# Kernel tuning notes

Measured on AMD Instinct MI355X. Metric: run time of the kernel, lower is better.

## Reference

```python
import jax, jax.numpy as jnp
import numpy as np

B, C, H, W = 16, 128, 128, 128
NUM_HEADS, HEAD_DIM = 4, 32
HIDDEN = NUM_HEADS * HEAD_DIM  # 128
GROUPS = 32
EPS = 1e-5


def setup_inputs() -> dict:
    key = jax.random.key(0)
    ks = jax.random.split(key, 6)
    # conv1x1 weights: torch Conv2d weight (out, in, 1, 1) -> stored as (out, in)
    fan_qkv = C
    fan_proj = HIDDEN
    return {
        "x": jax.random.normal(ks[0], (B, C, H, W), dtype=jnp.float32),
        "gn_w": jnp.ones((C,), dtype=jnp.float32),
        "gn_b": jnp.zeros((C,), dtype=jnp.float32),
        "qkv_w": jax.random.normal(ks[1], (3 * HIDDEN, C), dtype=jnp.float32) / np.sqrt(fan_qkv),
        "proj_w": jax.random.normal(ks[2], (C, HIDDEN), dtype=jnp.float32) / np.sqrt(fan_proj),
        "proj_b": jax.random.normal(ks[3], (C,), dtype=jnp.float32) * 0.01,
    }


def reference(x, gn_w, gn_b, qkv_w, proj_w, proj_b):
    b, c, h, w = x.shape
    n = h * w
    residual = x
    # GroupNorm(32 groups), biased variance, affine
    xg = x.reshape(b, GROUPS, c // GROUPS, h, w)
    mu = xg.mean(axis=(2, 3, 4), keepdims=True)
    var = xg.var(axis=(2, 3, 4), keepdims=True)
    xn = ((xg - mu) * jax.lax.rsqrt(var + EPS)).reshape(b, c, h, w)
    xn = xn * gn_w[None, :, None, None] + gn_b[None, :, None, None]
    # 1x1 conv QKV (no bias); channel layout -> (b, 3, heads, head_dim, n)
    qkv = jnp.einsum('oc,bchw->bohw', qkv_w, xn)
    qkv = qkv.reshape(b, 3, NUM_HEADS, HEAD_DIM, n)
    q, k, v = qkv[:, 0], qkv[:, 1], qkv[:, 2]
    q = jax.nn.softmax(q, axis=-1)   # over spatial positions
    k = jax.nn.softmax(k, axis=-2)   # over head_dim
    # context = k @ v^T : (b,h,D,D)
    ctx = jnp.einsum('bhdn,bhen->bhde', k, v)
    # out = context^T @ q : (b,h,D,n)
    out = jnp.einsum('bhde,bhdn->bhen', ctx, q)
    out = out.reshape(b, HIDDEN, h, w)
    # 1x1 conv projection (with bias)
    out = jnp.einsum('co,bohw->bchw', proj_w, out) + proj_b[None, :, None, None]
    return out + residual
```

## Files before the change

### kernel.cpp

```cpp
#include <hip/hip_runtime.h>


#define B_ 16
#define C_ 128
#define N_ 16384

typedef short bf16x8 __attribute__((ext_vector_type(8)));
typedef float f32x4 __attribute__((ext_vector_type(4)));
typedef unsigned u32x2 __attribute__((ext_vector_type(2)));

__device__ __forceinline__ ushort f2bf(float f) {
    union { float f; unsigned u; } v; v.f = f;
    unsigned r = (v.u + 0x7FFFu + ((v.u >> 16) & 1u)) >> 16;
    return (ushort)r;
}
__device__ __forceinline__ float bf2f(unsigned h) {
    union { unsigned u; float f; } v; v.u = h << 16;
    return v.f;
}

__global__ void k_stats(const float* __restrict__ x, const float* __restrict__ gnw,
                        const float* __restrict__ gnb, float* __restrict__ sc,
                        float* __restrict__ bi,
                        const float* __restrict__ qkvw, ushort* __restrict__ wbf) {
    int bg = blockIdx.x;
    if (bg >= 512) {
        int i = (bg - 512) * 1024 + threadIdx.x;
        if (i < 384 * 128) wbf[i] = f2bf(qkvw[i]);
        return;
    }
    const float4* p = (const float4*)(x + (size_t)bg * (4 * N_));
    float s = 0.f, s2 = 0.f;
    for (int i = threadIdx.x; i < N_; i += 1024) {
        float4 v = p[i];
        s  += v.x + v.y + v.z + v.w;
        s2 += v.x * v.x + v.y * v.y + v.z * v.z + v.w * v.w;
    }
    #pragma unroll
    for (int d = 32; d > 0; d >>= 1) { s += __shfl_xor(s, d); s2 += __shfl_xor(s2, d); }
    __shared__ float ls[16], ls2[16];
    int wid = threadIdx.x >> 6, lane = threadIdx.x & 63;
    if (lane == 0) { ls[wid] = s; ls2[wid] = s2; }
    __syncthreads();
    if (threadIdx.x == 0) {
        float S = 0.f, S2 = 0.f;
        #pragma unroll
        for (int i = 0; i < 16; ++i) { S += ls[i]; S2 += ls2[i]; }
        float m = S / 65536.f;
        float var = S2 / 65536.f - m * m;
        float rs = rsqrtf(var + 1e-5f);
        int b = bg >> 5, g = bg & 31;
        #pragma unroll
        for (int i = 0; i < 4; ++i) {
            int c = g * 4 + i;
            float scv = rs * gnw[c];
            sc[b * 128 + c] = scv;
            bi[b * 128 + c] = gnb[c] - m * scv;
        }
    }
}


#define MFMA16(A, Bv, Cc) __builtin_amdgcn_mfma_f32_16x16x32_bf16(A, Bv, Cc, 0, 0, 0)

#define DO_Q(J) do { \
    f32x4 acc = {0.f, 0.f, 0.f, 0.f}; \
    acc = MFMA16(wf[J][0], xb[0], acc); acc = MFMA16(wf[J][1], xb[1], acc); \
    acc = MFMA16(wf[J][2], xb[2], acc); acc = MFMA16(wf[J][3], xb[3], acc); \
    qacc[J][0] += __expf(acc[0]); qacc[J][1] += __expf(acc[1]); \
    qacc[J][2] += __expf(acc[2]); qacc[J][3] += __expf(acc[3]); \
} while (0)

#define DO_K(JLO, H) do { \
    f32x4 aL = {0.f, 0.f, 0.f, 0.f}, aH = {0.f, 0.f, 0.f, 0.f}; \
    aL = MFMA16(wf[JLO][0], xb[0], aL);     aH = MFMA16(wf[(JLO)+1][0], xb[0], aH); \
    aL = MFMA16(wf[JLO][1], xb[1], aL);     aH = MFMA16(wf[(JLO)+1][1], xb[1], aH); \
    aL = MFMA16(wf[JLO][2], xb[2], aL);     aH = MFMA16(wf[(JLO)+1][2], xb[2], aH); \
    aL = MFMA16(wf[JLO][3], xb[3], aL);     aH = MFMA16(wf[(JLO)+1][3], xb[3], aH); \
    float eL0 = __expf(aL[0]), eL1 = __expf(aL[1]), eL2 = __expf(aL[2]), eL3 = __expf(aL[3]); \
    float eH0 = __expf(aH[0]), eH1 = __expf(aH[1]), eH2 = __expf(aH[2]), eH3 = __expf(aH[3]); \
    float s = eL0 + eL1 + eL2 + eL3 + eH0 + eH1 + eH2 + eH3; \
    s += __shfl_xor(s, 16); s += __shfl_xor(s, 32); \
    float rinv = 1.f / s; \
    ksm[H][lg * 4 + 0][nloc] = f2bf(eL0 * rinv); \
    ksm[H][lg * 4 + 1][nloc] = f2bf(eL1 * rinv); \
    ksm[H][lg * 4 + 2][nloc] = f2bf(eL2 * rinv); \
    ksm[H][lg * 4 + 3][nloc] = f2bf(eL3 * rinv); \
    ksm[H][16 + lg * 4 + 0][nloc] = f2bf(eH0 * rinv); \
    ksm[H][16 + lg * 4 + 1][nloc] = f2bf(eH1 * rinv); \
    ksm[H][16 + lg * 4 + 2][nloc] = f2bf(eH2 * rinv); \
    ksm[H][16 + lg * 4 + 3][nloc] = f2bf(eH3 * rinv); \
} while (0)

#define DO_V(J, HV, EB) do { \
    f32x4 acc = {0.f, 0.f, 0.f, 0.f}; \
    acc = MFMA16(wf[J][0], xb[0], acc); acc = MFMA16(wf[J][1], xb[1], acc); \
    acc = MFMA16(wf[J][2], xb[2], acc); acc = MFMA16(wf[J][3], xb[3], acc); \
    vls[HV][(EB) + lg * 4 + 0][nloc] = f2bf(acc[0]); \
    vls[HV][(EB) + lg * 4 + 1][nloc] = f2bf(acc[1]); \
    vls[HV][(EB) + lg * 4 + 2][nloc] = f2bf(acc[2]); \
    vls[HV][(EB) + lg * 4 + 3][nloc] = f2bf(acc[3]); \
} while (0)

__global__ __launch_bounds__(256, 2) void k_main(
    const float* __restrict__ x, const ushort* __restrict__ wbf,
    const float* __restrict__ scA, const float* __restrict__ biA,
    float* __restrict__ qsumP, float* __restrict__ ctxP) {
    int blk = blockIdx.x;
    int b = blk >> 6, nb = blk & 63;
    int tid = threadIdx.x, wid = tid >> 6, lane = tid & 63;
    int l15 = lane & 15, lg = lane >> 4;

    __shared__ __align__(16) ushort xs[4096];
    __shared__ __align__(16) ushort ksm[4][32][40];
    __shared__ __align__(16) ushort vls[4][32][40];

    bf16x8 wf[6][4];
    {
        const ushort* wr = wbf + (size_t)(wid * 96 + l15) * 128 + lg * 8;
        #pragma unroll
        for (int j = 0; j < 6; ++j)
            #pragma unroll
            for (int kc = 0; kc < 4; ++kc)
                wf[j][kc] = *(const bf16x8*)(wr + j * 2048 + kc * 32);
    }

    float qacc[6][4];
    #pragma unroll
    for (int j = 0; j < 6; ++j)
        #pragma unroll
        for (int r = 0; r < 4; ++r) qacc[j][r] = 0.f;
    f32x4 cacc[2][2];
    #pragma unroll
    for (int di = 0; di < 2; ++di)
        #pragma unroll
        for (int ei = 0; ei < 2; ++ei) cacc[di][ei] = (f32x4){0.f, 0.f, 0.f, 0.f};

    const int pk_ = tid & 7, pcb = tid >> 3;
    const float* xrow = x + (size_t)b * (C_ * N_) + nb * 256 + pk_ * 4;
    float scv[4], biv[4];
    #pragma unroll
    for (int i = 0; i < 4; ++i) {
        scv[i] = scA[b * 128 + pcb * 4 + i];
        biv[i] = biA[b * 128 + pcb * 4 + i];
    }
    unsigned boffj[4];
    #pragma unroll
    for (int j = 0; j < 4; ++j) {
        int n = pk_ * 4 + j;
        boffj[j] = (unsigned)(n * 256 + (((pcb >> 1) * 16) ^ ((n & 7) << 4)) + (pcb & 1) * 8);
    }

    float4 vbuf[4];
    #pragma unroll
    for (int i = 0; i < 4; ++i)
        vbuf[i] = *(const float4*)(xrow + (size_t)(pcb * 4 + i) * N_);

    for (int ch = 0; ch < 8; ++ch) {
        __syncthreads();
        unsigned e[4][4];
        #pragma unroll
        for (int i = 0; i < 4; ++i) {
            float s = scv[i], t = biv[i];
            e[i][0] = f2bf(vbuf[i].x * s + t);
            e[i][1] = f2bf(vbuf[i].y * s + t);
            e[i][2] = f2bf(vbuf[i].z * s + t);
            e[i][3] = f2bf(vbuf[i].w * s + t);
        }
        if (ch < 7) {
            #pragma unroll
            for (int i = 0; i < 4; ++i)
                vbuf[i] = *(const float4*)(xrow + (size_t)(pcb * 4 + i) * N_ + (ch + 1) * 32);
        }
        #pragma unroll
        for (int j = 0; j < 4; ++j) {
            u32x2 wj;
            wj.x = e[0][j] | (e[1][j] << 16);
            wj.y = e[2][j] | (e[3][j] << 16);
            *(u32x2*)((char*)xs + boffj[j]) = wj;
        }
        __syncthreads();

        #pragma unroll
        for (int nt = 0; nt < 2; ++nt) {
            int row = nt * 16 + l15;
            bf16x8 xb[4];
            #pragma unroll
            for (int kc = 0; kc < 4; ++kc) {
                unsigned off = (unsigned)(row * 256 +
                    (((kc * 4 + lg) * 16) ^ ((row & 7) << 4)));
                xb[kc] = *(const bf16x8*)((const char*)xs + off);
            }
            int nloc = nt * 16 + l15;

            if (wid == 0) {
                DO_Q(0); DO_Q(1); DO_Q(2); DO_Q(3); DO_Q(4); DO_Q(5);
            } else if (wid == 1) {
                DO_Q(0); DO_Q(1); DO_K(2, 0); DO_K(4, 1);
            } else if (wid == 2) {
                DO_K(0, 2); DO_K(2, 3); DO_V(4, 0, 0); DO_V(5, 0, 16);
            } else {
                DO_V(0, 1, 0); DO_V(1, 1, 16); DO_V(2, 2, 0);
                DO_V(3, 2, 16); DO_V(4, 3, 0); DO_V(5, 3, 16);
            }
        }
        __syncthreads();

        {
            bf16x8 A0 = *(const bf16x8*)&ksm[wid][l15][lg * 8];
            bf16x8 A1 = *(const bf16x8*)&ksm[wid][16 + l15][lg * 8];
            bf16x8 B0 = *(const bf16x8*)&vls[wid][l15][lg * 8];
            bf16x8 B1 = *(const bf16x8*)&vls[wid][16 + l15][lg * 8];
            cacc[0][0] = MFMA16(A0, B0, cacc[0][0]);
            cacc[0][1] = MFMA16(A0, B1, cacc[0][1]);
            cacc[1][0] = MFMA16(A1, B0, cacc[1][0]);
            cacc[1][1] = MFMA16(A1, B1, cacc[1][1]);
        }
    }

    int nq = (wid == 0) ? 6 : (wid == 1 ? 2 : 0);
    #pragma unroll
    for (int j = 0; j < 6; ++j) {
        if (j < nq) {
            #pragma unroll
            for (int r = 0; r < 4; ++r) {
                float s = qacc[j][r];
                s += __shfl_xor(s, 1); s += __shfl_xor(s, 2);
                s += __shfl_xor(s, 4); s += __shfl_xor(s, 8);
                if (l15 == 0)
                    qsumP[(size_t)blk * 128 + (wid * 6 + j) * 16 + lg * 4 + r] = s;
            }
        }
    }
    float* cp = ctxP + (size_t)blk * 4096 + wid * 1024;
    #pragma unroll
    for (int di = 0; di < 2; ++di)
        #pragma unroll
        for (int ei = 0; ei < 2; ++ei)
            #pragma unroll
            for (int r = 0; r < 4; ++r)
                cp[(di * 16 + lg * 4 + r) * 32 + ei * 16 + l15] = cacc[di][ei][r];
}

__global__ void k_red(float* __restrict__ ctxP) {
    int blk = blockIdx.x;
    int b = blk >> 3, sl = blk & 7;
    float* base = ctxP + (size_t)b * 64 * 4096;
    #pragma unroll
    for (int r = 0; r < 2; ++r) {
        int i = sl * 512 + r * 256 + threadIdx.x;
        float s = 0.f;
        for (int q = 0; q < 64; ++q) s += base[(size_t)q * 4096 + i];
        base[i] = s;
    }
}

__global__ void k_comb(const float* __restrict__ ctxP, const float* __restrict__ qsumP,
                       const float* __restrict__ projw, ushort* __restrict__ mpp) {
    int b = blockIdx.x, tid = threadIdx.x;
    __shared__ float ctx[4096];
    __shared__ float qinv[128];
    for (int i = tid; i < 4096; i += 256)
        ctx[i] = ctxP[(size_t)b * 64 * 4096 + i];
    if (tid < 128) {
        float s = 0.f;
        const float* p = qsumP + (size_t)b * 64 * 128 + tid;
        for (int q = 0; q < 64; ++q) s += p[q * 128];
        qinv[tid] = 1.f / s;
    }
    __syncthreads();
    int c = tid >> 1, hd0 = (tid & 1) * 64;
    unsigned ow[32];
    for (int k = 0; k < 64; ++k) {
        int hd = hd0 + k, h = hd >> 5, d = hd & 31;
        const float* pw = projw + c * 128 + h * 32;
        const float* cx = ctx + h * 1024 + d * 32;
        float s = 0.f;
        #pragma unroll 8
        for (int e = 0; e < 32; ++e) s += pw[e] * cx[e];
        s *= qinv[hd];
        ushort bv = f2bf(s);
        if (k & 1) ow[k >> 1] |= ((unsigned)bv) << 16; else ow[k >> 1] = bv;
    }
    ushort* dst = mpp + ((size_t)(b * 128 + c)) * 128 + hd0;
    #pragma unroll
    for (int q = 0; q < 8; ++q) {
        uint4 t; t.x = ow[q * 4]; t.y = ow[q * 4 + 1]; t.z = ow[q * 4 + 2]; t.w = ow[q * 4 + 3];
        ((uint4*)dst)[q] = t;
    }
}

__global__ __launch_bounds__(256) void k_final(
    const ushort* __restrict__ wbf, const ushort* __restrict__ mpp,
    const float* __restrict__ scA, const float* __restrict__ biA,
    const float* __restrict__ projb, const float* __restrict__ x,
    float* __restrict__ out) {
    int blk = blockIdx.x;
    int b = blk >> 8, nb = blk & 255;
    int tid = threadIdx.x, wid = tid >> 6, lane = tid & 63;
    int l15 = lane & 15, lg = lane >> 4;
    int n0 = nb * 64;

    __shared__ __align__(16) char lds[32768];
    ushort* xs   = (ushort*)lds;
    ushort* att  = (ushort*)lds;
    ushort* eqls = (ushort*)(lds + 16384);

    bf16x8 wq[2][4];
    #pragma unroll
    for (int j = 0; j < 2; ++j) {
        const ushort* wr = wbf + (size_t)((wid * 2 + j) * 16 + l15) * 128 + lg * 8;
        #pragma unroll
        for (int kc = 0; kc < 4; ++kc) wq[j][kc] = *(const bf16x8*)(wr + kc * 32);
    }
    bf16x8 bm[2][4];
    #pragma unroll
    for (int ctk = 0; ctk < 2; ++ctk) {
        const ushort* br = mpp + ((size_t)(b * 128 + (wid * 2 + ctk) * 16 + l15)) * 128 + lg * 8;
        #pragma unroll
        for (int kc = 0; kc < 4; ++kc) bm[ctk][kc] = *(const bf16x8*)(br + kc * 32);
    }

    const int pk_ = tid & 15, pcb = tid >> 4;
    float4 xv[8];
    {
        const float* xrow = x + (size_t)b * (C_ * N_) + n0 + pk_ * 4;
        unsigned e[8][4];
        #pragma unroll
        for (int i = 0; i < 8; ++i) {
            int c = pcb * 8 + i;
            float s = scA[b * 128 + c], t = biA[b * 128 + c];
            xv[i] = *(const float4*)(xrow + (size_t)c * N_);
            e[i][0] = f2bf(xv[i].x * s + t);
            e[i][1] = f2bf(xv[i].y * s + t);
            e[i][2] = f2bf(xv[i].z * s + t);
            e[i][3] = f2bf(xv[i].w * s + t);
        }
        #pragma unroll
        for (int j = 0; j < 4; ++j) {
            int n = pk_ * 4 + j;
            uint4 wj;
            wj.x = e[0][j] | (e[1][j] << 16);
            wj.y = e[2][j] | (e[3][j] << 16);
            wj.z = e[4][j] | (e[5][j] << 16);
            wj.w = e[6][j] | (e[7][j] << 16);
            unsigned byte = (unsigned)(n * 256 + ((pcb * 16) ^ ((n & 7) << 4)));
            *(uint4*)((char*)xs + byte) = wj;
        }
    }
    __syncthreads();

    #pragma unroll
    for (int nt = 0; nt < 4; ++nt) {
        int row = nt * 16 + l15;
        bf16x8 xb[4];
        #pragma unroll
        for (int kc = 0; kc < 4; ++kc) {
            unsigned off = (unsigned)(row * 256 + (((kc * 4 + lg) * 16) ^ ((row & 7) << 4)));
            xb[kc] = *(const bf16x8*)((const char*)xs + off);
        }
        #pragma unroll
        for (int j = 0; j < 2; ++j) {
            f32x4 a = {0.f, 0.f, 0.f, 0.f};
            #pragma unroll
            for (int kc = 0; kc < 4; ++kc) a = MFMA16(wq[j][kc], xb[kc], a);
            u32x2 pk;
            pk.x = (unsigned)f2bf(__expf(a[0])) | ((unsigned)f2bf(__expf(a[1])) << 16);
            pk.y = (unsigned)f2bf(__expf(a[2])) | ((unsigned)f2bf(__expf(a[3])) << 16);
            int ot = wid * 2 + j;
            unsigned byte = (unsigned)(row * 256 +
                (((ot * 2 + (lg >> 1)) * 16) ^ ((row & 7) << 4)) + (lg & 1) * 8);
            *(u32x2*)((char*)eqls + byte) = pk;
        }
    }
    __syncthreads();

    #pragma unroll
    for (int nt = 0; nt < 4; ++nt) {
        int row = nt * 16 + l15;
        bf16x8 af[4];
        #pragma unroll
        for (int kc = 0; kc < 4; ++kc) {
            unsigned off = (unsigned)(row * 256 + (((kc * 4 + lg) * 16) ^ ((row & 7) << 4)));
            af[kc] = *(const bf16x8*)((const char*)eqls + off);
        }
        #pragma unroll
        for (int ctk = 0; ctk < 2; ++ctk) {
            f32x4 a = {0.f, 0.f, 0.f, 0.f};
            #pragma unroll
            for (int kc = 0; kc < 4; ++kc) a = MFMA16(af[kc], bm[ctk][kc], a);
            int c = (wid * 2 + ctk) * 16 + l15;
            u32x2 pk;
            pk.x = (unsigned)f2bf(a[0]) | ((unsigned)f2bf(a[1]) << 16);
            pk.y = (unsigned)f2bf(a[2]) | ((unsigned)f2bf(a[3]) << 16);
            unsigned byte = (unsigned)(c * 128 +
                (((nt * 2 + (lg >> 1)) * 16) ^ ((c & 7) << 4)) + (lg & 1) * 8);
            *(u32x2*)((char*)att + byte) = pk;
        }
    }
    __syncthreads();

    {
        size_t obase = (size_t)b * (C_ * N_) + n0 + pk_ * 4;
        #pragma unroll
        for (int i = 0; i < 8; ++i) {
            int c = pcb * 8 + i;
            unsigned byte = (unsigned)(c * 128 +
                (((pk_ >> 1) * 16) ^ ((c & 7) << 4)) + (pk_ & 1) * 8);
            u32x2 pk = *(const u32x2*)((const char*)att + byte);
            float pbv = projb[c];
            f32x4 o4;
            o4[0] = bf2f(pk.x & 0xffffu) + pbv + xv[i].x;
            o4[1] = bf2f(pk.x >> 16)     + pbv + xv[i].y;
            o4[2] = bf2f(pk.y & 0xffffu) + pbv + xv[i].z;
            o4[3] = bf2f(pk.y >> 16)     + pbv + xv[i].w;
            *(f32x4*)(out + obase + (size_t)c * N_) = o4;
        }
    }
}

extern "C" void kernel_launch(void* const* d_in, const int* in_sizes, int n_in,
                              void* d_out, int out_size, void* d_ws, size_t ws_size,
                              hipStream_t stream) {
    const float* x     = (const float*)d_in[0];
    const float* gnw   = (const float*)d_in[1];
    const float* gnb   = (const float*)d_in[2];
    const float* qkvw  = (const float*)d_in[3];
    const float* projw = (const float*)d_in[4];
    const float* projb = (const float*)d_in[5];
    float* out = (float*)d_out;

    char* ws = (char*)d_ws;
    ushort* wbf   = (ushort*)(ws);
    float*  qsumP = (float*)(ws + 102400);
    ushort* mpp   = (ushort*)(ws + 626688);
    float*  sc    = (float*)(ws + 1150976);
    float*  bi    = (float*)(ws + 1159168);
    float*  ctxP  = (float*)(ws + 1167360);

    k_stats<<<560,  1024, 0, stream>>>(x, gnw, gnb, sc, bi, qkvw, wbf);
    k_main <<<1024, 256,  0, stream>>>(x, wbf, sc, bi, qsumP, ctxP);
    k_red  <<<128,  256,  0, stream>>>(ctxP);
    k_comb <<<16,   256,  0, stream>>>(ctxP, qsumP, projw, mpp);
    k_final<<<4096, 256,  0, stream>>>(wbf, mpp, sc, bi, projb, x, out);
}
```

Before: 211.5 us.

## Defer context MFMA past barrier and fold partial reduction into combine kernel

Moves the per-chunk K·V^T context MFMA to the start of the next chunk iteration, removing one block barrier per chunk in the main kernel. Merges the separate partial-context reduction kernel into the combine kernel, which now uses 1024 threads per batch to sum the 64 partials directly into shared memory. This saves a launch and a global round trip, but the reduction now runs on only 16 blocks, and removing the barrier risks a race on the shared staging buffer if it is not double-buffered.

```diff
diff --git a/kernel.cpp b/kernel.cpp
--- a/kernel.cpp
+++ b/kernel.cpp
@@ -102,6 +102,17 @@
     vls[HV][(EB) + lg * 4 + 3][nloc] = f2bf(acc[3]); \
 } while (0)
 
+#define DO_CTX() do { \
+    bf16x8 A0 = *(const bf16x8*)&ksm[wid][l15][lg * 8]; \
+    bf16x8 A1 = *(const bf16x8*)&ksm[wid][16 + l15][lg * 8]; \
+    bf16x8 B0 = *(const bf16x8*)&vls[wid][l15][lg * 8]; \
+    bf16x8 B1 = *(const bf16x8*)&vls[wid][16 + l15][lg * 8]; \
+    cacc[0][0] = MFMA16(A0, B0, cacc[0][0]); \
+    cacc[0][1] = MFMA16(A0, B1, cacc[0][1]); \
+    cacc[1][0] = MFMA16(A1, B0, cacc[1][0]); \
+    cacc[1][1] = MFMA16(A1, B1, cacc[1][1]); \
+} while (0)
+
 __global__ __launch_bounds__(256, 2) void k_main(
     const float* __restrict__ x, const ushort* __restrict__ wbf,
     const float* __restrict__ scA, const float* __restrict__ biA,
@@ -179,6 +190,7 @@
             wj.y = e[2][j] | (e[3][j] << 16);
             *(u32x2*)((char*)xs + boffj[j]) = wj;
         }
+        if (ch > 0) DO_CTX();
         __syncthreads();
 
         #pragma unroll
@@ -204,19 +216,9 @@
                 DO_V(3, 2, 16); DO_V(4, 3, 0); DO_V(5, 3, 16);
             }
         }
-        __syncthreads();
-
-        {
-            bf16x8 A0 = *(const bf16x8*)&ksm[wid][l15][lg * 8];
-            bf16x8 A1 = *(const bf16x8*)&ksm[wid][16 + l15][lg * 8];
-            bf16x8 B0 = *(const bf16x8*)&vls[wid][l15][lg * 8];
-            bf16x8 B1 = *(const bf16x8*)&vls[wid][16 + l15][lg * 8];
-            cacc[0][0] = MFMA16(A0, B0, cacc[0][0]);
-            cacc[0][1] = MFMA16(A0, B1, cacc[0][1]);
-            cacc[1][0] = MFMA16(A1, B0, cacc[1][0]);
-            cacc[1][1] = MFMA16(A1, B1, cacc[1][1]);
-        }
-    }
+    }
+    __syncthreads();
+    DO_CTX();
 
     int nq = (wid == 0) ? 6 : (wid == 1 ? 2 : 0);
     #pragma unroll
@@ -242,26 +244,20 @@
                 cp[(di * 16 + lg * 4 + r) * 32 + ei * 16 + l15] = cacc[di][ei][r];
 }
 
-__global__ void k_red(float* __restrict__ ctxP) {
-    int blk = blockIdx.x;
-    int b = blk >> 3, sl = blk & 7;
-    float* base = ctxP + (size_t)b * 64 * 4096;
-    #pragma unroll
-    for (int r = 0; r < 2; ++r) {
-        int i = sl * 512 + r * 256 + threadIdx.x;
-        float s = 0.f;
-        for (int q = 0; q < 64; ++q) s += base[(size_t)q * 4096 + i];
-        base[i] = s;
-    }
-}
-
-__global__ void k_comb(const float* __restrict__ ctxP, const float* __restrict__ qsumP,
-                       const float* __restrict__ projw, ushort* __restrict__ mpp) {
+__global__ __launch_bounds__(1024) void k_comb(
+    const float* __restrict__ ctxP, const float* __restrict__ qsumP,
+    const float* __restrict__ projw, ushort* __restrict__ mpp) {
     int b = blockIdx.x, tid = threadIdx.x;
     __shared__ float ctx[4096];
     __shared__ float qinv[128];
-    for (int i = tid; i < 4096; i += 256)
-        ctx[i] = ctxP[(size_t)b * 64 * 4096 + i];
+    const float* base = ctxP + (size_t)b * 64 * 4096;
+    #pragma unroll
+    for (int r = 0; r < 4; ++r) {
+        int i = r * 1024 + tid;
+        float s = 0.f;
+        for (int q = 0; q < 64; ++q) s += base[(size_t)q * 4096 + i];
+        ctx[i] = s;
+    }
     if (tid < 128) {
         float s = 0.f;
         const float* p = qsumP + (size_t)b * 64 * 128 + tid;
@@ -269,24 +265,27 @@
         qinv[tid] = 1.f / s;
     }
     __syncthreads();
-    int c = tid >> 1, hd0 = (tid & 1) * 64;
-    unsigned ow[32];
-    for (int k = 0; k < 64; ++k) {
-        int hd = hd0 + k, h = hd >> 5, d = hd & 31;
-        const float* pw = projw + c * 128 + h * 32;
-        const float* cx = ctx + h * 1024 + d * 32;
-        float s = 0.f;
-        #pragma unroll 8
-        for (int e = 0; e < 32; ++e) s += pw[e] * cx[e];
-        s *= qinv[hd];
-        ushort bv = f2bf(s);
-        if (k & 1) ow[k >> 1] |= ((unsigned)bv) << 16; else ow[k >> 1] = bv;
-    }
-    ushort* dst = mpp + ((size_t)(b * 128 + c)) * 128 + hd0;
-    #pragma unroll
-    for (int q = 0; q < 8; ++q) {
-        uint4 t; t.x = ow[q * 4]; t.y = ow[q * 4 + 1]; t.z = ow[q * 4 + 2]; t.w = ow[q * 4 + 3];
-        ((uint4*)dst)[q] = t;
+    if (tid < 256) {
+        int c = tid >> 1, hd0 = (tid & 1) * 64;
+        unsigned ow[32];
+        for (int k = 0; k < 64; ++k) {
+            int hd = hd0 + k, h = hd >> 5, d = hd & 31;
+            const float* pw = projw + c * 128 + h * 32;
+            const float* cx = ctx + h * 1024 + d * 32;
+            float s = 0.f;
+            #pragma unroll 8
+            for (int e = 0; e < 32; ++e) s += pw[e] * cx[e];
+            s *= qinv[hd];
+            ushort bv = f2bf(s);
+            if (k & 1) ow[k >> 1] |= ((unsigned)bv) << 16; else ow[k >> 1] = bv;
+        }
+        ushort* dst = mpp + ((size_t)(b * 128 + c)) * 128 + hd0;
+        #pragma unroll
+        for (int q = 0; q < 8; ++q) {
+            uint4 t; t.x = ow[q * 4]; t.y = ow[q * 4 + 1];
+            t.z = ow[q * 4 + 2]; t.w = ow[q * 4 + 3];
+            ((uint4*)dst)[q] = t;
+        }
     }
 }
 
@@ -440,7 +439,6 @@
 
     k_stats<<<560,  1024, 0, stream>>>(x, gnw, gnb, sc, bi, qkvw, wbf);
     k_main <<<1024, 256,  0, stream>>>(x, wbf, sc, bi, qsumP, ctxP);
-    k_red  <<<128,  256,  0, stream>>>(ctxP);
-    k_comb <<<16,   256,  0, stream>>>(ctxP, qsumP, projw, mpp);
+    k_comb <<<16,   1024, 0, stream>>>(ctxP, qsumP, projw, mpp);
     k_final<<<4096, 256,  0, stream>>>(wbf, mpp, sc, bi, projb, x, out);
 }
```

Measured after the change: 216.1 us. 1.02x slower.
